# Performance work log

Measured on AMD Instinct MI355X. Metric: run time of the kernel, lower is better.

The kernel has to match this reference:

```python
import jax, jax.numpy as jnp
import numpy as np

N_WORD = 50000
N_DOC = 10000
E_WW = 800000
E_WD = 320000


def _sage(h_src, h_dst, src, dst, n_dst, W_self, W_neigh, b):
    # DGL SAGEConv('mean'): fc_self(h_dst) + fc_neigh(mean_{u in N(v)} h_u) + bias
    ones = jnp.ones((src.shape[0],), dtype=h_src.dtype)
    deg = jax.ops.segment_sum(ones, dst, num_segments=n_dst)            # [n_dst]
    agg = jax.ops.segment_sum(h_src[src], dst, num_segments=n_dst)      # [n_dst, d]
    mean = agg / jnp.maximum(deg, 1.0)[:, None]                          # zero for isolated
    return h_dst @ W_self + mean @ W_neigh + b


def _layer(xw, xd, edges, Ws, Wn, b):
    (ww_s, ww_d, wwr_s, wwr_d, wd_s, wd_d, wdr_s, wdr_d) = edges
    # relations targeting 'word': word2word, word2wordr, word2documentr
    h_ww = _sage(xw, xw, ww_s, ww_d, N_WORD, Ws[0], Wn[0], b[0])
    h_wwr = _sage(xw, xw, wwr_s, wwr_d, N_WORD, Ws[1], Wn[1], b[1])
    h_wdr = _sage(xd, xw, wdr_s, wdr_d, N_WORD, Ws[3], Wn[3], b[3])
    # relation targeting 'document': word2document
    h_wd = _sage(xw, xd, wd_s, wd_d, N_DOC, Ws[2], Wn[2], b[2])
    # HeteroGraphConv aggregate='stack' then torch.sum(dim=1) == sum over relations; then relu
    return jax.nn.relu(h_ww + h_wwr + h_wdr), jax.nn.relu(h_wd)


def setup_inputs() -> dict:
    key = jax.random.key(0)
    ks = jax.random.split(key, 20)
    d_in, d_h = 256, 128
    inp = {
        "x_word": jax.random.normal(ks[0], (N_WORD, d_in), jnp.float32),
        "x_doc": jax.random.normal(ks[1], (N_DOC, d_in), jnp.float32),
        "ww_src": jax.random.randint(ks[2], (E_WW,), 0, N_WORD, jnp.int32),
        "ww_dst": jax.random.randint(ks[3], (E_WW,), 0, N_WORD, jnp.int32),
        "wwr_src": jax.random.randint(ks[4], (E_WW,), 0, N_WORD, jnp.int32),
        "wwr_dst": jax.random.randint(ks[5], (E_WW,), 0, N_WORD, jnp.int32),
        "wd_src": jax.random.randint(ks[6], (E_WD,), 0, N_WORD, jnp.int32),
        "wd_dst": jax.random.randint(ks[7], (E_WD,), 0, N_DOC, jnp.int32),
        "wdr_src": jax.random.randint(ks[8], (E_WD,), 0, N_DOC, jnp.int32),
        "wdr_dst": jax.random.randint(ks[9], (E_WD,), 0, N_WORD, jnp.int32),
        "Wself1": jax.random.normal(ks[10], (4, d_in, d_h), jnp.float32) * (1.0 / np.sqrt(d_in)),
        "Wneigh1": jax.random.normal(ks[11], (4, d_in, d_h), jnp.float32) * (1.0 / np.sqrt(d_in)),
        "b1": jnp.zeros((4, d_h), jnp.float32),
        "Wself2": jax.random.normal(ks[12], (4, d_h, d_h), jnp.float32) * (1.0 / np.sqrt(d_h)),
        "Wneigh2": jax.random.normal(ks[13], (4, d_h, d_h), jnp.float32) * (1.0 / np.sqrt(d_h)),
        "b2": jnp.zeros((4, d_h), jnp.float32),
        "lin_w": jax.random.normal(ks[14], (1, d_h), jnp.float32) * (1.0 / np.sqrt(d_h)),
        "lin_b": jnp.ones((1,), jnp.float32),
    }
    return inp


def reference(x_word, x_doc, ww_src, ww_dst, wwr_src, wwr_dst, wd_src, wd_dst,
              wdr_src, wdr_dst, Wself1, Wneigh1, b1, Wself2, Wneigh2, b2, lin_w, lin_b):
    edges = (ww_src, ww_dst, wwr_src, wwr_dst, wd_src, wd_dst, wdr_src, wdr_dst)
    xw, xd = _layer(x_word, x_doc, edges, Wself1, Wneigh1, b1)
    xw, xd = _layer(xw, xd, edges, Wself2, Wneigh2, b2)
    out_w = jax.nn.sigmoid(xw @ lin_w.T + lin_b)  # [N_WORD, 1]
    out_d = jax.nn.sigmoid(xd @ lin_w.T + lin_b)  # [N_DOC, 1]
    return out_w, out_d
```

## Files before the change

### kernel.cpp

```cpp
#include <hip/hip_runtime.h>
#include <math.h>

#define N_WORD 50000
#define N_DOC  10000
#define E_WW   800000
#define E_WD   320000
#define D_IN   256
#define D_H    128

#define NPB    1024
#define NBK_W  49
#define NBK_D  10
#define BKT    (3 * NBK_W + NBK_D)
#define EPB    4096
#define NBLK_WW 196
#define NBLK_WD 79
#define NBLK_TOT (2 * NBLK_WW + 2 * NBLK_WD)
#define PACK_BLKS 145

#define CAP_WW  18432
#define CAP_WDR 8192
#define CAP_WD  34816

#define WSTRIP ((N_WORD + 63) / 64)
#define DSTRIP ((N_DOC + 63) / 64)
#define NSTRIP (WSTRIP + DSTRIP)

typedef __attribute__((ext_vector_type(8))) short short8;
typedef __attribute__((ext_vector_type(4))) float f32x4;

__device__ inline unsigned short f2bf(float f) {
  unsigned u = __float_as_uint(f);
  u = (u + 0x7fffu + ((u >> 16) & 1u)) >> 16;
  return (unsigned short)u;
}

struct G6 { const short* B[6]; unsigned short* C[6]; };

template <int ABF, int K>
__device__ void gemm_body(const void* __restrict__ Aw, const void* __restrict__ Ad,
                          const G6& g, int blk) {
  constexpr int KT = K >> 5;
  int wid = threadIdx.x >> 6, lane = threadIdx.x & 63;
  const void* A; int M, row0, h0, h1;
  if (blk < WSTRIP) { A = Aw; M = N_WORD; row0 = blk << 6; h0 = 0; h1 = 4; }
  else { A = Ad; M = N_DOC; row0 = (blk - WSTRIP) << 6; h0 = 4; h1 = 6; }
  int r = lane & 15, quad = lane >> 4;
  int m0 = row0 + wid * 16;
  int mA = m0 + r; if (mA >= M) mA = M - 1;
  short8 afr[KT];
  if (ABF) {
    const short* ap = (const short*)A + (size_t)mA * K + quad * 8;
#pragma unroll
    for (int kt = 0; kt < KT; ++kt) afr[kt] = *(const short8*)(ap + kt * 32);
  } else {
    const float* ap = (const float*)A + (size_t)mA * K + quad * 8;
#pragma unroll
    for (int kt = 0; kt < KT; ++kt) {
      float4 a0 = *(const float4*)(ap + kt * 32);
      float4 a1 = *(const float4*)(ap + kt * 32 + 4);
      short8 v;
      v[0] = (short)f2bf(a0.x); v[1] = (short)f2bf(a0.y);
      v[2] = (short)f2bf(a0.z); v[3] = (short)f2bf(a0.w);
      v[4] = (short)f2bf(a1.x); v[5] = (short)f2bf(a1.y);
      v[6] = (short)f2bf(a1.z); v[7] = (short)f2bf(a1.w);
      afr[kt] = v;
    }
  }
  for (int h = h0; h < h1; ++h) {
    const short* Bp = g.B[h];
    f32x4 acc[8];
#pragma unroll
    for (int nt = 0; nt < 8; ++nt) acc[nt] = (f32x4){0.f, 0.f, 0.f, 0.f};
#pragma unroll
    for (int kt = 0; kt < KT; ++kt) {
      const short* bbase = Bp + ((size_t)kt * 4096) + lane * 8;
#pragma unroll
      for (int nt = 0; nt < 8; ++nt) {
        short8 bf = *(const short8*)(bbase + (size_t)nt * 512);
        acc[nt] = __builtin_amdgcn_mfma_f32_16x16x32_bf16(afr[kt], bf, acc[nt], 0, 0, 0);
      }
    }
    unsigned short* C = g.C[h];
#pragma unroll
    for (int nt = 0; nt < 8; ++nt)
#pragma unroll
      for (int rr = 0; rr < 4; ++rr) {
        int row = m0 + quad * 4 + rr;
        if (row < M) C[(size_t)row * 128 + nt * 16 + r] = f2bf(acc[nt][rr]);
      }
  }
}

struct CSRB {
  const unsigned *st_ww, *st_wwr, *st_wdr, *st_wd;
  unsigned short *c_ww, *c_wwr, *c_wdr, *c_wd;
  int *rp_ww, *rp_wwr, *rp_wdr, *rp_wd;
  const int* bcnt;
};

__device__ void place_body(int g, const CSRB& q, int* smem) {
  int* cnt = smem;
  int* off = cnt + NPB;
  int* sm  = off + NPB;
  int* s_b = sm + 256;
  const unsigned* st; unsigned short* csr; int* rp; int relFirst, relLast, n, cap, Etot;
  if (g < NBK_W)            { st = q.st_ww;  csr = q.c_ww;  rp = q.rp_ww;  relFirst = 0;         relLast = NBK_W - 1;     n = N_WORD; cap = CAP_WW;  Etot = E_WW; }
  else if (g < 2 * NBK_W)   { st = q.st_wwr; csr = q.c_wwr; rp = q.rp_wwr; relFirst = NBK_W;     relLast = 2 * NBK_W - 1; n = N_WORD; cap = CAP_WW;  Etot = E_WW; }
  else if (g < 3 * NBK_W)   { st = q.st_wdr; csr = q.c_wdr; rp = q.rp_wdr; relFirst = 2 * NBK_W; relLast = 3 * NBK_W - 1; n = N_WORD; cap = CAP_WDR; Etot = E_WD; }
  else                      { st = q.st_wd;  csr = q.c_wd;  rp = q.rp_wd;  relFirst = 3 * NBK_W; relLast = BKT - 1;       n = N_DOC;  cap = CAP_WD;  Etot = E_WD; }
  int cb = g - relFirst;
  int tid = threadIdx.x;
  if (tid < 64) {
    int v = (tid < cb) ? q.bcnt[relFirst + tid] : 0;
#pragma unroll
    for (int o = 32; o > 0; o >>= 1) v += __shfl_xor(v, o);
    if (tid == 0) s_b[0] = v;
  }
  if (g == relLast && tid == 65) rp[n] = Etot;
  int node_base = cb << 10;
  int node_cnt = n - node_base; if (node_cnt > NPB) node_cnt = NPB;
  int ecnt = q.bcnt[g];
  const unsigned* w = st + (size_t)cb * cap;
  for (int i = tid; i < NPB; i += 256) cnt[i] = 0;
  __syncthreads();
  int bstart = s_b[0];
  for (int j = tid; j < ecnt; j += 256) atomicAdd(&cnt[w[j] >> 16], 1);
  __syncthreads();
  int c[4], s = 0;
#pragma unroll
  for (int jj = 0; jj < 4; ++jj) { c[jj] = cnt[tid * 4 + jj]; s += c[jj]; }
  sm[tid] = s;
  __syncthreads();
  for (int o = 1; o < 256; o <<= 1) {
    int add = (tid >= o) ? sm[tid - o] : 0;
    __syncthreads();
    sm[tid] += add;
    __syncthreads();
  }
  int ex = sm[tid] - s;
#pragma unroll
  for (int jj = 0; jj < 4; ++jj) { off[tid * 4 + jj] = ex; ex += c[jj]; }
  __syncthreads();
#pragma unroll
  for (int jj = 0; jj < 4; ++jj) {
    int i = tid * 4 + jj;
    if (i < node_cnt) rp[node_base + i] = bstart + off[i];
  }
  __syncthreads();
  for (int j = tid; j < ecnt; j += 256) {
    unsigned e = w[j];
    int p = atomicAdd(&off[e >> 16], 1);
    csr[bstart + p] = (unsigned short)(e & 0xFFFFu);
  }
}

__global__ __launch_bounds__(256, 4) void gemm1_place(
    const float* __restrict__ Aw, const float* __restrict__ Ad, G6 g, CSRB q) {
  __shared__ int smem[NPB * 2 + 256 + 1];
  if (blockIdx.x < BKT) place_body(blockIdx.x, q, smem);
  else gemm_body<0, 256>(Aw, Ad, g, blockIdx.x - BKT);
}

__global__ __launch_bounds__(256, 4) void gemm2_kernel(
    const void* __restrict__ Aw, const void* __restrict__ Ad, G6 g) {
  gemm_body<1, 128>(Aw, Ad, g, blockIdx.x);
}

__device__ inline void rel_map(int b, const int* wwd, const int* wwrd, const int* wdrd,
                               const int* wdd, const int*& dst, int& E, int& gbase, int& lb) {
  if (b < NBLK_WW) { dst = wwd; E = E_WW; gbase = 0; lb = b; }
  else if (b < 2 * NBLK_WW) { dst = wwrd; E = E_WW; gbase = NBK_W; lb = b - NBLK_WW; }
  else if (b < 2 * NBLK_WW + NBLK_WD) { dst = wdrd; E = E_WD; gbase = 2 * NBK_W; lb = b - 2 * NBLK_WW; }
  else { dst = wdd; E = E_WD; gbase = 3 * NBK_W; lb = b - 2 * NBLK_WW - NBLK_WD; }
}

__global__ __launch_bounds__(256) void binpack_kernel(
    const int* wws, const int* wwd, const int* wwrs, const int* wwrd,
    const int* wdrs, const int* wdrd, const int* wds, const int* wdd,
    int* bcnt, unsigned* st_ww, unsigned* st_wwr, unsigned* st_wdr, unsigned* st_wd,
    const float* __restrict__ Ws1, const float* __restrict__ Wn1,
    const float* __restrict__ Ws2, const float* __restrict__ Wn2,
    short* __restrict__ Bp1, short* __restrict__ Bp2,
    const float* __restrict__ b1, const float* __restrict__ b2,
    float* __restrict__ bs1, float* __restrict__ bs2) {
  int b = blockIdx.x;
  if (b >= NBLK_TOT) {
    int tid = (b - NBLK_TOT) * 256 + threadIdx.x;
    const int L1T = 6 * 4096;
    const int L2T = 6 * 2048;
    if (tid >= L1T + L2T) {
      int t = tid - (L1T + L2T);
      if (t < 128) bs1[t] = b1[t] + b1[128 + t] + b1[384 + t];
      else if (t < 256) { int u = t - 128; bs2[u] = b2[u] + b2[128 + u] + b2[384 + u]; }
      return;
    }
    const float *src0, *src1 = nullptr, *src2 = nullptr;
    short* dstp;
    int kt, nt, lane;
    if (tid < L1T) {
      int mat = tid / 4096, rem = tid % 4096;
      kt = rem / 512; nt = (rem / 64) % 8; lane = rem % 64;
      const int W1 = 256 * 128;
      if (mat == 0) { src0 = Ws1; src1 = Ws1 + W1; src2 = Ws1 + 3 * W1; }
      else if (mat <= 4) src0 = Wn1 + (size_t)(mat - 1) * W1;
      else src0 = Ws1 + 2 * W1;
      dstp = Bp1 + (size_t)mat * W1 + ((size_t)(kt * 8 + nt) * 64 + lane) * 8;
    } else {
      int t2 = tid - L1T;
      int mat = t2 / 2048, rem = t2 % 2048;
      kt = rem / 512; nt = (rem / 64) % 8; lane = rem % 64;
      const int W2 = 128 * 128;
      if (mat == 0) { src0 = Ws2; src1 = Ws2 + W2; src2 = Ws2 + 3 * W2; }
      else if (mat <= 4) src0 = Wn2 + (size_t)(mat - 1) * W2;
      else src0 = Ws2 + 2 * W2;
      dstp = Bp2 + (size_t)mat * W2 + ((size_t)(kt * 8 + nt) * 64 + lane) * 8;
    }
    int n = nt * 16 + (lane & 15);
    int kb = kt * 32 + (lane >> 4) * 8;
    short8 v;
#pragma unroll
    for (int j = 0; j < 8; ++j) {
      float f = src0[(size_t)(kb + j) * 128 + n];
      if (src1) f += src1[(size_t)(kb + j) * 128 + n] + src2[(size_t)(kb + j) * 128 + n];
      v[j] = (short)f2bf(f);
    }
    *(short8*)dstp = v;
    return;
  }
  __shared__ int h[4][64], wb[4][64], cur[4][64];
  const int* dst; int E, gbase, lb;
  rel_map(b, wwd, wwrd, wdrd, wdd, dst, E, gbase, lb);
  const int* src; unsigned* st; int cap;
  if (b < NBLK_WW) { src = wws; st = st_ww; cap = CAP_WW; }
  else if (b < 2 * NBLK_WW) { src = wwrs; st = st_wwr; cap = CAP_WW; }
  else if (b < 2 * NBLK_WW + NBLK_WD) { src = wdrs; st = st_wdr; cap = CAP_WDR; }
  else { src = wds; st = st_wd; cap = CAP_WD; }
  int tid = threadIdx.x;
  int wave = tid >> 6;
  ((int*)h)[tid] = 0;
  ((int*)cur)[tid] = 0;
  __syncthreads();
  int e0 = lb * EPB;
#pragma unroll
  for (int k = 0; k < EPB / 256; ++k) {
    int i = e0 + k * 256 + tid;
    if (i < E) atomicAdd(&h[wave][dst[i] >> 10], 1);
  }
  __syncthreads();
  if (tid < NBK_W) {
    int t0 = h[0][tid], t1 = h[1][tid], t2 = h[2][tid], t3 = h[3][tid];
    int tot = t0 + t1 + t2 + t3;
    int base = tot ? atomicAdd(&bcnt[gbase + tid], tot) : 0;
    wb[0][tid] = base;
    wb[1][tid] = base + t0;
    wb[2][tid] = base + t0 + t1;
    wb[3][tid] = base + t0 + t1 + t2;
  }
  __syncthreads();
#pragma unroll
  for (int k = 0; k < EPB / 256; ++k) {
    int i = e0 + k * 256 + tid;
    if (i < E) {
      int d = dst[i];
      int bk = d >> 10;
      int l = atomicAdd(&cur[wave][bk], 1);
      st[(size_t)bk * cap + wb[wave][bk] + l] =
          (unsigned)(src[i] & 0xFFFF) | ((unsigned)(d & (NPB - 1)) << 16);
    }
  }
}

__device__ inline void accum_rel(const unsigned* __restrict__ y,
                                 const unsigned short* __restrict__ csr,
                                 int beg, int end, int lane, float& f0, float& f1) {
  float a0 = 0.f, a1 = 0.f;
  for (int base = beg; base < end; base += 64) {
    int cnt = end - base; if (cnt > 64) cnt = 64;
    int ld = base + lane; if (ld >= end) ld = end - 1;
    int idx = csr[ld];
    int j = 0;
    for (; j + 7 < cnt; j += 8) {
      unsigned u[8];
#pragma unroll
      for (int k = 0; k < 8; ++k) {
        int s = __builtin_amdgcn_readlane(idx, j + k);
        u[k] = y[((size_t)s << 6) + lane];
      }
#pragma unroll
      for (int k = 0; k < 8; ++k) {
        a0 += __uint_as_float(u[k] << 16);
        a1 += __uint_as_float(u[k] & 0xffff0000u);
      }
    }
    for (; j < cnt; ++j) {
      int s = __builtin_amdgcn_readlane(idx, j);
      unsigned uu = y[((size_t)s << 6) + lane];
      a0 += __uint_as_float(uu << 16);
      a1 += __uint_as_float(uu & 0xffff0000u);
    }
  }
  int deg = end - beg;
  float inv = 1.0f / (float)(deg > 1 ? deg : 1);
  f0 += a0 * inv;
  f1 += a1 * inv;
}

__global__ __launch_bounds__(256) void gather_all(
    const unsigned* __restrict__ y_ww, const unsigned* __restrict__ y_wwr,
    const unsigned* __restrict__ y_wdr, const unsigned* __restrict__ y_wd,
    const unsigned short* __restrict__ c_ww, const unsigned short* __restrict__ c_wwr,
    const unsigned short* __restrict__ c_wdr, const unsigned short* __restrict__ c_wd,
    const int* __restrict__ r_ww, const int* __restrict__ r_wwr,
    const int* __restrict__ r_wdr, const int* __restrict__ r_wd,
    const unsigned* __restrict__ tW, const unsigned* __restrict__ tD,
    const float* __restrict__ bW, const float* __restrict__ bD,
    const float* __restrict__ lw, const float* __restrict__ lb,
    unsigned* __restrict__ oW16, unsigned* __restrict__ oD16,
    float* __restrict__ oF, int mode) {
  int gn = (blockIdx.x << 2) + (threadIdx.x >> 6);
  if (gn >= N_WORD + N_DOC) return;
  int lane = threadIdx.x & 63;
  float f0, f1;
  if (gn < N_WORD) {
    int node = gn;
    unsigned tu = tW[((size_t)node << 6) + lane];
    f0 = __uint_as_float(tu << 16);
    f1 = __uint_as_float(tu & 0xffff0000u);
    accum_rel(y_ww, c_ww, r_ww[node], r_ww[node + 1], lane, f0, f1);
    accum_rel(y_wwr, c_wwr, r_wwr[node], r_wwr[node + 1], lane, f0, f1);
    accum_rel(y_wdr, c_wdr, r_wdr[node], r_wdr[node + 1], lane, f0, f1);
    float2 bv = ((const float2*)bW)[lane];
    f0 = fmaxf(f0 + bv.x, 0.f);
    f1 = fmaxf(f1 + bv.y, 0.f);
    if (mode == 1) {
      oW16[((size_t)node << 6) + lane] = (unsigned)f2bf(f0) | ((unsigned)f2bf(f1) << 16);
    } else {
      float2 lv = ((const float2*)lw)[lane];
      float s = f0 * lv.x + f1 * lv.y;
#pragma unroll
      for (int off = 32; off > 0; off >>= 1) s += __shfl_xor(s, off);
      if (lane == 0) oF[node] = 1.0f / (1.0f + expf(-(s + lb[0])));
    }
  } else {
    int node = gn - N_WORD;
    unsigned tu = tD[((size_t)node << 6) + lane];
    f0 = __uint_as_float(tu << 16);
    f1 = __uint_as_float(tu & 0xffff0000u);
    accum_rel(y_wd, c_wd, r_wd[node], r_wd[node + 1], lane, f0, f1);
    float2 bv = ((const float2*)bD)[lane];
    f0 = fmaxf(f0 + bv.x, 0.f);
    f1 = fmaxf(f1 + bv.y, 0.f);
    if (mode == 1) {
      oD16[((size_t)node << 6) + lane] = (unsigned)f2bf(f0) | ((unsigned)f2bf(f1) << 16);
    } else {
      float2 lv = ((const float2*)lw)[lane];
      float s = f0 * lv.x + f1 * lv.y;
#pragma unroll
      for (int off = 32; off > 0; off >>= 1) s += __shfl_xor(s, off);
      if (lane == 0) oF[N_WORD + node] = 1.0f / (1.0f + expf(-(s + lb[0])));
    }
  }
}

extern "C" void kernel_launch(void* const* d_in, const int* in_sizes, int n_in,
                              void* d_out, int out_size, void* d_ws, size_t ws_size,
                              hipStream_t stream) {
  const float* xw      = (const float*)d_in[0];
  const float* xd      = (const float*)d_in[1];
  const int*   ww_src  = (const int*)d_in[2];
  const int*   ww_dst  = (const int*)d_in[3];
  const int*   wwr_src = (const int*)d_in[4];
  const int*   wwr_dst = (const int*)d_in[5];
  const int*   wd_src  = (const int*)d_in[6];
  const int*   wd_dst  = (const int*)d_in[7];
  const int*   wdr_src = (const int*)d_in[8];
  const int*   wdr_dst = (const int*)d_in[9];
  const float* Ws1     = (const float*)d_in[10];
  const float* Wn1     = (const float*)d_in[11];
  const float* b1      = (const float*)d_in[12];
  const float* Ws2     = (const float*)d_in[13];
  const float* Wn2     = (const float*)d_in[14];
  const float* b2      = (const float*)d_in[15];
  const float* lin_w   = (const float*)d_in[16];
  const float* lin_b   = (const float*)d_in[17];
  float* out = (float*)d_out;

  char* p = (char*)d_ws;
  auto alloc = [&](size_t nbytes) {
    char* r = p;
    p += (nbytes + 255) & ~(size_t)255;
    return r;
  };
  unsigned* twA  = (unsigned*)alloc((size_t)N_WORD * D_H * 2);
  unsigned* tdA  = (unsigned*)alloc((size_t)N_DOC * D_H * 2);
  unsigned* xw1B = (unsigned*)alloc((size_t)N_WORD * D_H * 2);
  unsigned* xd1B = (unsigned*)alloc((size_t)N_DOC * D_H * 2);
  unsigned* yB0 = (unsigned*)alloc((size_t)N_WORD * D_H * 2);
  unsigned* yB1 = (unsigned*)alloc((size_t)N_WORD * D_H * 2);
  unsigned* yB2 = (unsigned*)alloc((size_t)N_WORD * D_H * 2);
  unsigned* ydB = (unsigned*)alloc((size_t)N_DOC * D_H * 2);
  unsigned short* csr_ww  = (unsigned short*)alloc((size_t)E_WW * 2);
  unsigned short* csr_wwr = (unsigned short*)alloc((size_t)E_WW * 2);
  unsigned short* csr_wdr = (unsigned short*)alloc((size_t)E_WD * 2);
  unsigned short* csr_wd  = (unsigned short*)alloc((size_t)E_WD * 2);
  int* rp_ww  = (int*)alloc((size_t)(N_WORD + 1) * 4);
  int* rp_wwr = (int*)alloc((size_t)(N_WORD + 1) * 4);
  int* rp_wdr = (int*)alloc((size_t)(N_WORD + 1) * 4);
  int* rp_wd  = (int*)alloc((size_t)(N_DOC + 1) * 4);
  short* Bp1 = (short*)alloc((size_t)6 * 256 * 128 * 2);
  short* Bp2 = (short*)alloc((size_t)6 * 128 * 128 * 2);
  int* bcnt  = (int*)alloc((size_t)BKT * 4);
  float* bs1 = (float*)alloc(D_H * 4);
  float* bs2 = (float*)alloc(D_H * 4);
  unsigned* yBX = (unsigned*)alloc((size_t)N_WORD * D_H * 2);
  unsigned* st_ww  = yB0;
  unsigned* st_wwr = st_ww + (size_t)NBK_W * CAP_WW;
  unsigned* st_wdr = yB1;
  unsigned* st_wd  = st_wdr + (size_t)NBK_W * CAP_WDR;

  hipMemsetAsync(bcnt, 0, BKT * 4, stream);
  binpack_kernel<<<NBLK_TOT + PACK_BLKS, 256, 0, stream>>>(
      ww_src, ww_dst, wwr_src, wwr_dst, wdr_src, wdr_dst, wd_src, wd_dst,
      bcnt, st_ww, st_wwr, st_wdr, st_wd,
      Ws1, Wn1, Ws2, Wn2, Bp1, Bp2, b1, b2, bs1, bs2);

  const int W1 = 256 * 128;
  const int W2 = 128 * 128;

  G6 g1;
  g1.B[0] = Bp1 + 0 * W1; g1.C[0] = (unsigned short*)twA;
  g1.B[1] = Bp1 + 1 * W1; g1.C[1] = (unsigned short*)yB2;
  g1.B[2] = Bp1 + 2 * W1; g1.C[2] = (unsigned short*)xw1B;
  g1.B[3] = Bp1 + 3 * W1; g1.C[3] = (unsigned short*)yBX;
  g1.B[4] = Bp1 + 5 * W1; g1.C[4] = (unsigned short*)tdA;
  g1.B[5] = Bp1 + 4 * W1; g1.C[5] = (unsigned short*)ydB;
  CSRB q;
  q.st_ww = st_ww; q.st_wwr = st_wwr; q.st_wdr = st_wdr; q.st_wd = st_wd;
  q.c_ww = csr_ww; q.c_wwr = csr_wwr; q.c_wdr = csr_wdr; q.c_wd = csr_wd;
  q.rp_ww = rp_ww; q.rp_wwr = rp_wwr; q.rp_wdr = rp_wdr; q.rp_wd = rp_wd;
  q.bcnt = bcnt;
  gemm1_place<<<BKT + NSTRIP, 256, 0, stream>>>(xw, xd, g1, q);
  gather_all<<<(N_WORD + N_DOC + 3) / 4, 256, 0, stream>>>(
      yB2, xw1B, ydB, yBX, csr_ww, csr_wwr, csr_wdr, csr_wd,
      rp_ww, rp_wwr, rp_wdr, rp_wd, twA, tdA, bs1, b1 + 256,
      lin_w, lin_b, yB0, xd1B, nullptr, 1);

  G6 g2;
  g2.B[0] = Bp2 + 0 * W2; g2.C[0] = (unsigned short*)twA;
  g2.B[1] = Bp2 + 1 * W2; g2.C[1] = (unsigned short*)yB2;
  g2.B[2] = Bp2 + 2 * W2; g2.C[2] = (unsigned short*)xw1B;
  g2.B[3] = Bp2 + 3 * W2; g2.C[3] = (unsigned short*)yBX;
  g2.B[4] = Bp2 + 5 * W2; g2.C[4] = (unsigned short*)tdA;
  g2.B[5] = Bp2 + 4 * W2; g2.C[5] = (unsigned short*)ydB;
  gemm2_kernel<<<NSTRIP, 256, 0, stream>>>(yB0, xd1B, g2);
  gather_all<<<(N_WORD + N_DOC + 3) / 4, 256, 0, stream>>>(
      yB2, xw1B, ydB, yBX, csr_ww, csr_wwr, csr_wdr, csr_wd,
      rp_ww, rp_wwr, rp_wdr, rp_wd, twA, tdA, bs2, b2 + 256,
      lin_w, lin_b, nullptr, nullptr, out, 2);
}
```

Before: 428.7 us.

## Shrink CSR placement buckets from 1024 to 256 nodes

```diff
diff --git a/kernel.cpp b/kernel.cpp
--- a/kernel.cpp
+++ b/kernel.cpp
@@ -8,9 +8,9 @@
 #define D_IN   256
 #define D_H    128
 
-#define NPB    1024
-#define NBK_W  49
-#define NBK_D  10
+#define NPB    256
+#define NBK_W  196
+#define NBK_D  40
 #define BKT    (3 * NBK_W + NBK_D)
 #define EPB    4096
 #define NBLK_WW 196
@@ -18,9 +18,9 @@
 #define NBLK_TOT (2 * NBLK_WW + 2 * NBLK_WD)
 #define PACK_BLKS 145
 
-#define CAP_WW  18432
-#define CAP_WDR 8192
-#define CAP_WD  34816
+#define CAP_WW  4736
+#define CAP_WDR 2176
+#define CAP_WD  8960
 
 #define WSTRIP ((N_WORD + 63) / 64)
 #define DSTRIP ((N_DOC + 63) / 64)
@@ -101,9 +101,8 @@
 
 __device__ void place_body(int g, const CSRB& q, int* smem) {
   int* cnt = smem;
-  int* off = cnt + NPB;
-  int* sm  = off + NPB;
-  int* s_b = sm + 256;
+  int* off = cnt + 256;
+  int* sm  = off + 256;
   const unsigned* st; unsigned short* csr; int* rp; int relFirst, relLast, n, cap, Etot;
   if (g < NBK_W)            { st = q.st_ww;  csr = q.c_ww;  rp = q.rp_ww;  relFirst = 0;         relLast = NBK_W - 1;     n = N_WORD; cap = CAP_WW;  Etot = E_WW; }
   else if (g < 2 * NBK_W)   { st = q.st_wwr; csr = q.c_wwr; rp = q.rp_wwr; relFirst = NBK_W;     relLast = 2 * NBK_W - 1; n = N_WORD; cap = CAP_WW;  Etot = E_WW; }
@@ -111,26 +110,26 @@
   else                      { st = q.st_wd;  csr = q.c_wd;  rp = q.rp_wd;  relFirst = 3 * NBK_W; relLast = BKT - 1;       n = N_DOC;  cap = CAP_WD;  Etot = E_WD; }
   int cb = g - relFirst;
   int tid = threadIdx.x;
-  if (tid < 64) {
-    int v = (tid < cb) ? q.bcnt[relFirst + tid] : 0;
-#pragma unroll
-    for (int o = 32; o > 0; o >>= 1) v += __shfl_xor(v, o);
-    if (tid == 0) s_b[0] = v;
-  }
-  if (g == relLast && tid == 65) rp[n] = Etot;
-  int node_base = cb << 10;
+  int v = (tid < cb) ? q.bcnt[relFirst + tid] : 0;
+  sm[tid] = v;
+  __syncthreads();
+  for (int o = 128; o > 0; o >>= 1) {
+    if (tid < o) sm[tid] += sm[tid + o];
+    __syncthreads();
+  }
+  int bstart = sm[0];
+  if (g == relLast && tid == 0) rp[n] = Etot;
+  __syncthreads();
+  int node_base = cb << 8;
   int node_cnt = n - node_base; if (node_cnt > NPB) node_cnt = NPB;
   int ecnt = q.bcnt[g];
   const unsigned* w = st + (size_t)cb * cap;
-  for (int i = tid; i < NPB; i += 256) cnt[i] = 0;
-  __syncthreads();
-  int bstart = s_b[0];
+  cnt[tid] = 0;
+  __syncthreads();
   for (int j = tid; j < ecnt; j += 256) atomicAdd(&cnt[w[j] >> 16], 1);
   __syncthreads();
-  int c[4], s = 0;
-#pragma unroll
-  for (int jj = 0; jj < 4; ++jj) { c[jj] = cnt[tid * 4 + jj]; s += c[jj]; }
-  sm[tid] = s;
+  int c = cnt[tid];
+  sm[tid] = c;
   __syncthreads();
   for (int o = 1; o < 256; o <<= 1) {
     int add = (tid >= o) ? sm[tid - o] : 0;
@@ -138,15 +137,9 @@
     sm[tid] += add;
     __syncthreads();
   }
-  int ex = sm[tid] - s;
-#pragma unroll
-  for (int jj = 0; jj < 4; ++jj) { off[tid * 4 + jj] = ex; ex += c[jj]; }
-  __syncthreads();
-#pragma unroll
-  for (int jj = 0; jj < 4; ++jj) {
-    int i = tid * 4 + jj;
-    if (i < node_cnt) rp[node_base + i] = bstart + off[i];
-  }
+  int ex = sm[tid] - c;
+  off[tid] = ex;
+  if (tid < node_cnt) rp[node_base + tid] = bstart + ex;
   __syncthreads();
   for (int j = tid; j < ecnt; j += 256) {
     unsigned e = w[j];
@@ -157,7 +150,7 @@
 
 __global__ __launch_bounds__(256, 4) void gemm1_place(
     const float* __restrict__ Aw, const float* __restrict__ Ad, G6 g, CSRB q) {
-  __shared__ int smem[NPB * 2 + 256 + 1];
+  __shared__ int smem[768];
   if (blockIdx.x < BKT) place_body(blockIdx.x, q, smem);
   else gemm_body<0, 256>(Aw, Ad, g, blockIdx.x - BKT);
 }
@@ -184,6 +177,7 @@
     short* __restrict__ Bp1, short* __restrict__ Bp2,
     const float* __restrict__ b1, const float* __restrict__ b2,
     float* __restrict__ bs1, float* __restrict__ bs2) {
+  __shared__ int h[4][NBK_W], wb[4][NBK_W], cur[4][NBK_W];
   int b = blockIdx.x;
   if (b >= NBLK_TOT) {
     int tid = (b - NBLK_TOT) * 256 + threadIdx.x;
@@ -228,7 +222,6 @@
     *(short8*)dstp = v;
     return;
   }
-  __shared__ int h[4][64], wb[4][64], cur[4][64];
   const int* dst; int E, gbase, lb;
   rel_map(b, wwd, wwrd, wdrd, wdd, dst, E, gbase, lb);
   const int* src; unsigned* st; int cap;
@@ -238,14 +231,13 @@
   else { src = wds; st = st_wd; cap = CAP_WD; }
   int tid = threadIdx.x;
   int wave = tid >> 6;
-  ((int*)h)[tid] = 0;
-  ((int*)cur)[tid] = 0;
+  for (int i = tid; i < 4 * NBK_W; i += 256) { ((int*)h)[i] = 0; ((int*)cur)[i] = 0; }
   __syncthreads();
   int e0 = lb * EPB;
 #pragma unroll
   for (int k = 0; k < EPB / 256; ++k) {
     int i = e0 + k * 256 + tid;
-    if (i < E) atomicAdd(&h[wave][dst[i] >> 10], 1);
+    if (i < E) atomicAdd(&h[wave][dst[i] >> 8], 1);
   }
   __syncthreads();
   if (tid < NBK_W) {
@@ -263,7 +255,7 @@
     int i = e0 + k * 256 + tid;
     if (i < E) {
       int d = dst[i];
-      int bk = d >> 10;
+      int bk = d >> 8;
       int l = atomicAdd(&cur[wave][bk], 1);
       st[(size_t)bk * cap + wb[wave][bk] + l] =
           (unsigned)(src[i] & 0xFFFF) | ((unsigned)(d & (NPB - 1)) << 16);
```

New measurement: 402.9 us. 6.0% less time.
